# Optimization experiments

Measured on AMD Instinct MI355X. Metric: run time of the kernel, lower is better.

## Reference

```python
import jax, jax.numpy as jnp
import numpy as np

N_NODES = 50000
N_FEAT = 128
HID = 64
N_EDGES = 1600000
RK4_STEPS = 2
LN_EPS = 1e-5


def setup_inputs() -> dict:
    key = jax.random.key(0)
    ks = jax.random.split(key, 16)
    s = 1.0 / np.sqrt(HID)
    se = 1.0 / np.sqrt(N_FEAT)
    return {
        "x": jax.random.normal(ks[0], (N_NODES, N_FEAT), dtype=jnp.float32),
        "edge_index_pos": jax.random.randint(ks[1], (2, N_EDGES), 0, N_NODES, dtype=jnp.int64),
        "edge_index_neg": jax.random.randint(ks[2], (2, N_EDGES), 0, N_NODES, dtype=jnp.int64),
        "t": jnp.arange(2, dtype=jnp.float32),
        "W_enc": jax.random.uniform(ks[3], (HID, N_FEAT), jnp.float32, -se, se),
        "b_enc": jax.random.uniform(ks[4], (HID,), jnp.float32, -se, se),
        "W_pos": jax.random.uniform(ks[5], (HID, HID), jnp.float32, -s, s),
        "b_pos": jax.random.uniform(ks[6], (HID,), jnp.float32, -s, s),
        "W_neg": jax.random.uniform(ks[7], (HID, HID), jnp.float32, -s, s),
        "b_neg": jax.random.uniform(ks[8], (HID,), jnp.float32, -s, s),
        "W_psi_pos": jax.random.uniform(ks[9], (HID, HID), jnp.float32, -s, s),
        "b_psi_pos": jax.random.uniform(ks[10], (HID,), jnp.float32, -s, s),
        "W_psi_neg": jax.random.uniform(ks[11], (HID, HID), jnp.float32, -s, s),
        "b_psi_neg": jax.random.uniform(ks[12], (HID,), jnp.float32, -s, s),
        "ln_gamma": jnp.ones((HID,), jnp.float32),
        "ln_beta": jnp.zeros((HID,), jnp.float32),
    }


def _layer_norm(h, gamma, beta):
    mu = jnp.mean(h, axis=-1, keepdims=True)
    var = jnp.mean(jnp.square(h - mu), axis=-1, keepdims=True)
    return (h - mu) * jax.lax.rsqrt(var + LN_EPS) * gamma + beta


def _gcn_conv(h, W, b, src, dst, n_nodes):
    # PyG GCNConv: add self-loops, symmetric normalization D^-1/2 (A+I) D^-1/2 (X W^T) + b
    x = h @ W.T                                   # [N, HID]
    loops = jnp.arange(n_nodes, dtype=src.dtype)
    src_f = jnp.concatenate([src, loops])
    dst_f = jnp.concatenate([dst, loops])
    deg = jax.ops.segment_sum(jnp.ones_like(dst_f, dtype=x.dtype), dst_f, num_segments=n_nodes)
    dinv = jax.lax.rsqrt(deg)                     # deg >= 1 due to self-loops
    norm = dinv[src_f] * dinv[dst_f]              # [E+N]
    msg = norm[:, None] * x[src_f]                # gather
    return jax.ops.segment_sum(msg, dst_f, num_segments=n_nodes) + b


def _ode_func(h, ep, en, p):
    hn = _layer_norm(h, p["ln_gamma"], p["ln_beta"])
    h_pos = _gcn_conv(hn, p["W_pos"], p["b_pos"], ep[0], ep[1], hn.shape[0])
    h_neg = _gcn_conv(hn, p["W_neg"], p["b_neg"], en[0], en[1], hn.shape[0])
    # dropout is identity in eval mode
    delta = (h_pos @ p["W_psi_pos"].T + p["b_psi_pos"]) + (h_neg @ p["W_psi_neg"].T + p["b_psi_neg"])
    return jnp.clip(delta, -50.0, 50.0)


def reference(x, edge_index_pos, edge_index_neg, t,
              W_enc, b_enc, W_pos, b_pos, W_neg, b_neg,
              W_psi_pos, b_psi_pos, W_psi_neg, b_psi_neg, ln_gamma, ln_beta):
    p = dict(W_pos=W_pos, b_pos=b_pos, W_neg=W_neg, b_neg=b_neg,
             W_psi_pos=W_psi_pos, b_psi_pos=b_psi_pos, W_psi_neg=W_psi_neg,
             b_psi_neg=b_psi_neg, ln_gamma=ln_gamma, ln_beta=ln_beta)
    h = x @ W_enc.T + b_enc
    dt = (t[1] - t[0]) / RK4_STEPS
    f = lambda hh: _ode_func(hh, edge_index_pos, edge_index_neg, p)
    for _ in range(RK4_STEPS):  # fixed-step RK4 (stands in for odeint dopri5)
        k1 = f(h)
        k2 = f(h + 0.5 * dt * k1)
        k3 = f(h + 0.5 * dt * k2)
        k4 = f(h + dt * k3)
        h = h + (dt / 6.0) * (k1 + 2.0 * k2 + 2.0 * k3 + k4)
    return h
```

## Files before the change

### kernel.cpp

```cpp
#include <hip/hip_runtime.h>

#define N_NODES 50000
#define N_FEAT  128
#define HID     64
#define N_EDGES 1600000
#define LN_EPS  1e-5f
#define NB2     400
#define BW2     125
#define CAP2    5120u

typedef unsigned int uint;
typedef unsigned short ushort;
typedef _Float16 h2 __attribute__((ext_vector_type(2)));

#if __has_builtin(__builtin_amdgcn_fdot2)
#define FDOT2(a,b,c) __builtin_amdgcn_fdot2((a),(b),(c),false)
#else
#define FDOT2(a,b,c) ((float)(a)[0]*(float)(b)[0] + (float)(a)[1]*(float)(b)[1] + (c))
#endif

__device__ __forceinline__ float bcastf(float v, int l){
  return __uint_as_float(__builtin_amdgcn_readlane(__float_as_uint(v), l));
}
__device__ __forceinline__ h2 h2x(h2 a, int m){
  return __builtin_bit_cast(h2, __shfl_xor(__builtin_bit_cast(int, a), m));
}
__device__ __forceinline__ ushort f16u(float f){
  return __builtin_bit_cast(ushort, (_Float16)f);
}
__device__ __forceinline__ h2 wdup(uint e){
  return __builtin_bit_cast(h2, (e & 0xFFFF0000u) | (e >> 16));
}
__device__ __forceinline__ h2 wdup16(uint d){
  return __builtin_bit_cast(h2, d | (d << 16));
}
__device__ __forceinline__ void fma4(h2* a, uint4 v, h2 w){
  a[0] += w * __builtin_bit_cast(h2, v.x);
  a[1] += w * __builtin_bit_cast(h2, v.y);
  a[2] += w * __builtin_bit_cast(h2, v.z);
  a[3] += w * __builtin_bit_cast(h2, v.w);
}
__device__ __forceinline__ uint4 ldrow(const ushort* __restrict__ xs, uint r, int rowoff){
  return *(const uint4*)(xs + (size_t)r * HID + rowoff);
}

__global__ void prep_kernel(const float* __restrict__ Wpp, const float* __restrict__ Wp,
                            const float* __restrict__ Wpn, const float* __restrict__ Wn,
                            const float* __restrict__ bp, const float* __restrict__ bpp,
                            const float* __restrict__ bn, const float* __restrict__ bpn,
                            ushort* __restrict__ Wc16_p, ushort* __restrict__ Wc16_n,
                            float* __restrict__ bc,
                            ushort* __restrict__ hn16a, ushort* __restrict__ hn16b){
  int idx = blockIdx.x * blockDim.x + threadIdx.x;
  if (idx < 4096){
    int j = idx >> 6, k = idx & 63;
    float sp = 0.f, sn = 0.f;
    for (int m = 0; m < 64; ++m){
      sp += Wpp[j * 64 + m] * Wp[m * 64 + k];
      sn += Wpn[j * 64 + m] * Wn[m * 64 + k];
    }
    Wc16_p[idx] = f16u(sp); Wc16_n[idx] = f16u(sn);
  } else if (idx < 4160){
    int j = idx - 4096;
    float s = bpp[j] + bpn[j];
    for (int m = 0; m < 64; ++m) s += Wpp[j * 64 + m] * bp[m] + Wpn[j * 64 + m] * bn[m];
    bc[j] = s;
  } else if (idx < 4224){
    int q = idx - 4160;
    hn16a[(size_t)N_NODES * HID + q] = 0;
    hn16b[(size_t)N_NODES * HID + q] = 0;
  }
}

__global__ __launch_bounds__(256) void binA_kernel(
    const int* __restrict__ ep, const int* __restrict__ en,
    uint* __restrict__ bin_cur, uint* __restrict__ recs_p, uint* __restrict__ recs_n){
  __shared__ uint sh[8192];
  __shared__ uint cnt2[NB2], gb2[NB2], rnk2[NB2];
  const int NBLK = (N_EDGES + 8191) / 8192;
  int bid = blockIdx.x;
  int side = bid >= NBLK;
  const int* e = side ? en : ep;
  uint* recs = side ? recs_n : recs_p;
  uint* bcur = bin_cur + side * NB2;
  int cbase = (side ? bid - NBLK : bid) * 8192;
  int tid = threadIdx.x;
  for (int i = tid; i < NB2; i += 256){ cnt2[i] = 0; rnk2[i] = 0; }
  __syncthreads();
  for (int i = tid; i < 8192; i += 256){
    int t = cbase + i;
    uint r = 0xFFFFFFFFu;
    if (t < N_EDGES){
      uint s = (uint)e[t], d = (uint)e[N_EDGES + t];
      r = (d << 16) | s;
      atomicAdd(&cnt2[d / BW2], 1u);
    }
    sh[i] = r;
  }
  __syncthreads();
  for (int i = tid; i < NB2; i += 256) gb2[i] = atomicAdd(&bcur[i], cnt2[i]);
  __syncthreads();
  for (int i = tid; i < 8192; i += 256){
    uint r = sh[i];
    if (r != 0xFFFFFFFFu){
      uint b = (r >> 16) / BW2;
      uint pos = gb2[b] + atomicAdd(&rnk2[b], 1u);
      recs[b * CAP2 + pos] = r;
    }
  }
}

__global__ __launch_bounds__(256) void fillC_kernel(
    const uint* __restrict__ bin_cur,
    const uint* __restrict__ recs_p, const uint* __restrict__ recs_n,
    int* __restrict__ cnt_p, int* __restrict__ cnt_n,
    float* __restrict__ dinv_p, float* __restrict__ dinv_n,
    ushort* __restrict__ d16p, ushort* __restrict__ d16n,
    ushort* __restrict__ cs_p, ushort* __restrict__ cs_n){
  __shared__ int hist[128];
  __shared__ int curx[128];
  __shared__ ushort staged[CAP2];
  __shared__ uint base_s;
  int bid = blockIdx.x;
  int side = bid >= NB2; int b = side ? bid - NB2 : bid;
  const uint* recs = (side ? recs_n : recs_p) + (size_t)b * CAP2;
  int* cnt = side ? cnt_n : cnt_p;
  float* dinv = side ? dinv_n : dinv_p;
  ushort* d16 = side ? d16n : d16p;
  ushort* cs = side ? cs_n : cs_p;
  int tid = threadIdx.x, lane = tid & 63, wid = tid >> 6;
  int nodebase = b * BW2;
  if (tid < 128) hist[tid] = 0;
  __syncthreads();
  uint n = bin_cur[side * NB2 + b];
  if (wid == 1){
    uint s = 0;
    for (int k = lane; k < b; k += 64) s += bin_cur[side * NB2 + k];
    #pragma unroll
    for (int d = 1; d < 64; d <<= 1) s += __shfl_xor(s, d);
    if (lane == 0) base_s = s;
  }
  for (uint i = tid; i < n; i += 256)
    atomicAdd(&hist[(recs[i] >> 16) - nodebase], 1);
  __syncthreads();
  if (tid < BW2){
    int c = hist[tid];
    cnt[nodebase + tid] = c;
    float dv = rsqrtf((float)(c + 1));
    dinv[nodebase + tid] = dv;
    d16[nodebase + tid] = f16u(dv);
  }
  if (wid == 0){
    int carry = 0;
    #pragma unroll
    for (int base = 0; base < BW2; base += 64){
      int idx = base + lane;
      int v = (idx < BW2) ? hist[idx] : 0;
      int x = v;
      #pragma unroll
      for (int d = 1; d < 64; d <<= 1){
        int y = __shfl_up(x, d);
        if (lane >= d) x += y;
      }
      if (idx < BW2) curx[idx] = carry + x - v;
      int tot = __shfl(x, 63);
      carry = carry + tot;
    }
  }
  __syncthreads();
  for (uint i = tid; i < n; i += 256){
    uint r = recs[i];
    int d = (int)(r >> 16) - nodebase;
    int p = atomicAdd(&curx[d], 1);
    staged[p] = (ushort)(r & 0xFFFFu);
  }
  __syncthreads();
  uint base = base_s;
  for (uint i = tid; i < n; i += 256) cs[base + i] = staged[i];
}

__global__ __launch_bounds__(1024) void scan16_kernel(
    const uint* __restrict__ bin_cur,
    const int* __restrict__ c0, int* __restrict__ o0,
    const int* __restrict__ c1, int* __restrict__ o1){
  __shared__ int wsum[16];
  __shared__ int wexcl[16];
  __shared__ int carry_s;
  int side = blockIdx.x >> 3, b = blockIdx.x & 7;
  const int* c = side ? c1 : c0;
  int* o = side ? o1 : o0;
  int tid = threadIdx.x, lane = tid & 63, wid = tid >> 6;
  if (wid == 0){
    int s = 0;
    for (int k = lane; k < 50 * b; k += 64) s += (int)bin_cur[side * NB2 + k];
    #pragma unroll
    for (int d = 1; d < 64; d <<= 1) s += __shfl_xor(s, d);
    if (lane == 0) carry_s = s;
  }
  __syncthreads();
  int lo = b * 6250, hi = lo + 6250;
  for (int base = lo; base < hi; base += 1024){
    int idx = base + tid;
    int v = (idx < hi) ? c[idx] : 0;
    int x = v;
    #pragma unroll
    for (int d = 1; d < 64; d <<= 1){
      int y = __shfl_up(x, d);
      if (lane >= d) x += y;
    }
    if (lane == 63) wsum[wid] = x;
    __syncthreads();
    int block_total = 0;
    if (tid == 0){
      int s = 0;
      for (int wv = 0; wv < 16; ++wv){ wexcl[wv] = s; s += wsum[wv]; }
      block_total = s;
    }
    __syncthreads();
    if (idx < hi) o[idx] = carry_s + wexcl[wid] + (x - v);
    __syncthreads();
    if (tid == 0) carry_s += block_total;
    __syncthreads();
  }
  if (b == 7 && tid == 0) o[N_NODES] = carry_s;
}

__global__ __launch_bounds__(256) void pack_kernel(
    const ushort* __restrict__ cs_p, const ushort* __restrict__ cs_n,
    const ushort* __restrict__ d16p, const ushort* __restrict__ d16n,
    uint* __restrict__ cs32_p, uint* __restrict__ cs32_n){
  int i = blockIdx.x * 256 + threadIdx.x;
  if (i < N_EDGES){
    uint s = cs_p[i];
    cs32_p[i] = ((uint)d16p[s] << 16) | s;
  } else if (i < 2 * N_EDGES){
    int k = i - N_EDGES;
    uint s = cs_n[k];
    cs32_n[k] = ((uint)d16n[s] << 16) | s;
  }
}

__global__ __launch_bounds__(256) void enc_kernel(
    const float* __restrict__ x, const float* __restrict__ Wenc, const float* __restrict__ benc,
    const float* __restrict__ gamma, const float* __restrict__ beta,
    float* __restrict__ hbase, ushort* __restrict__ hn16){
  int lane = threadIdx.x & 63, wid = threadIdx.x >> 6;
  float we[128];
  const float* wr = Wenc + lane * N_FEAT;
  #pragma unroll
  for (int k4 = 0; k4 < 32; ++k4){
    float4 v = *(const float4*)(wr + 4 * k4);
    we[4*k4] = v.x; we[4*k4+1] = v.y; we[4*k4+2] = v.z; we[4*k4+3] = v.w;
  }
  float bv = benc[lane], g = gamma[lane], bt = beta[lane];
  int gw = blockIdx.x * 4 + wid, nw = gridDim.x * 4;
  for (int p = gw; p < N_NODES / 2; p += nw){
    int n0 = 2 * p, n1 = n0 + 1;
    float xa0 = x[(size_t)n0 * N_FEAT + lane], xb0 = x[(size_t)n0 * N_FEAT + 64 + lane];
    float xa1 = x[(size_t)n1 * N_FEAT + lane], xb1 = x[(size_t)n1 * N_FEAT + 64 + lane];
    float h0 = bv, h1 = bv;
    #pragma unroll
    for (int k = 0; k < 64; ++k){
      h0 += bcastf(xa0, k) * we[k];
      h1 += bcastf(xa1, k) * we[k];
      h0 += bcastf(xb0, k) * we[64 + k];
      h1 += bcastf(xb1, k) * we[64 + k];
    }
    hbase[n0 * HID + lane] = h0;
    hbase[n1 * HID + lane] = h1;
    float s0 = h0, q0 = h0 * h0, s1 = h1, q1 = h1 * h1;
    #pragma unroll
    for (int d = 1; d < 64; d <<= 1){
      s0 += __shfl_xor(s0, d); q0 += __shfl_xor(q0, d);
      s1 += __shfl_xor(s1, d); q1 += __shfl_xor(q1, d);
    }
    float mu0 = s0 * (1.0f/64.0f), var0 = q0 * (1.0f/64.0f) - mu0 * mu0;
    float mu1 = s1 * (1.0f/64.0f), var1 = q1 * (1.0f/64.0f) - mu1 * mu1;
    hn16[n0 * HID + lane] = f16u((h0 - mu0) * rsqrtf(var0 + LN_EPS) * g + bt);
    hn16[n1 * HID + lane] = f16u((h1 - mu1) * rsqrtf(var1 + LN_EPS) * g + bt);
  }
}

__device__ __forceinline__ void gather_side_acc(
    const ushort* __restrict__ hn16, const uint* __restrict__ cs32,
    int s0, int s1, int g, int rowoff, int lane, h2* acc){
  for (int base = s0; base < s1; base += 64){
    int jj = base + lane;
    uint e = (jj < s1) ? cs32[jj] : (uint)N_NODES;
    int cnt = min(64, s1 - base);
    int nt = (cnt + 7) >> 3;
    for (int t = 0; t < nt; ++t){
      uint ee = (uint)__shfl((int)e, 8 * t + g);
      fma4(acc, ldrow(hn16, ee & 0xFFFFu, rowoff), wdup(ee));
    }
  }
}

__global__ __launch_bounds__(256) void gather2_kernel(
    const ushort* __restrict__ hn16,
    const uint* __restrict__ cs32_p, const int* __restrict__ off_p,
    const float* __restrict__ dinv_p, const ushort* __restrict__ d16p,
    const uint* __restrict__ cs32_n, const int* __restrict__ off_n,
    const float* __restrict__ dinv_n, const ushort* __restrict__ d16n,
    const ushort* __restrict__ Wc16_p, const ushort* __restrict__ Wc16_n,
    const float* __restrict__ bc, const float* __restrict__ gamma, const float* __restrict__ beta,
    const float* __restrict__ tvec,
    float* __restrict__ hbase, float* __restrict__ acc, ushort* __restrict__ hn16o,
    int st, int emit){
  int lane = threadIdx.x & 63, wid = threadIdx.x >> 6;
  int pair = blockIdx.x * 4 + wid;
  int nA = 2 * pair, nB = nA + 1;
  if (nA >= N_NODES) return;
  int g = lane >> 3, rowoff = 8 * (lane & 7);

  int pA0 = off_p[nA], pA1 = off_p[nA + 1], pB1 = off_p[nB + 1];
  int qA0 = off_n[nA], qA1 = off_n[nA + 1], qB1 = off_n[nB + 1];
  int dPA = pA1 - pA0, dPB = pB1 - pA1, dNA = qA1 - qA0, dNB = qB1 - qA1;

  h2 aPA[4] = {h2{0,0},h2{0,0},h2{0,0},h2{0,0}};
  h2 aPB[4] = {h2{0,0},h2{0,0},h2{0,0},h2{0,0}};
  h2 aNA[4] = {h2{0,0},h2{0,0},h2{0,0},h2{0,0}};
  h2 aNB[4] = {h2{0,0},h2{0,0},h2{0,0},h2{0,0}};

  {
    uint4 rA = ldrow(hn16, (g==0)?(uint)nA:(uint)N_NODES, rowoff);
    uint4 rB = ldrow(hn16, (g==0)?(uint)nB:(uint)N_NODES, rowoff);
    uint dpA = d16p[nA], dnA = d16n[nA], dpB = d16p[nB], dnB = d16n[nB];
    fma4(aPA, rA, wdup16(dpA)); fma4(aNA, rA, wdup16(dnA));
    fma4(aPB, rB, wdup16(dpB)); fma4(aNB, rB, wdup16(dnB));
  }

  if (dPA <= 64 && dPB <= 64 && dNA <= 64 && dNB <= 64){
    uint ePA = (lane < dPA) ? cs32_p[pA0 + lane] : (uint)N_NODES;
    uint ePB = (lane < dPB) ? cs32_p[pA1 + lane] : (uint)N_NODES;
    uint eNA = (lane < dNA) ? cs32_n[qA0 + lane] : (uint)N_NODES;
    uint eNB = (lane < dNB) ? cs32_n[qA1 + lane] : (uint)N_NODES;
    int dP = dPA > dPB ? dPA : dPB;
    int dN = dNA > dNB ? dNA : dNB;
    int dM = dP > dN ? dP : dN;
    int ntM = (dM + 7) >> 3;
    for (int t = 0; t < ntM; t += 2){
      int gi0 = 8 * t + g, gi1 = gi0 + 8;
      uint uPA0 = (uint)__shfl((int)ePA, gi0), uPA1 = (uint)__shfl((int)ePA, gi1);
      uint uPB0 = (uint)__shfl((int)ePB, gi0), uPB1 = (uint)__shfl((int)ePB, gi1);
      uint uNA0 = (uint)__shfl((int)eNA, gi0), uNA1 = (uint)__shfl((int)eNA, gi1);
      uint uNB0 = (uint)__shfl((int)eNB, gi0), uNB1 = (uint)__shfl((int)eNB, gi1);
      uint4 vPA0 = ldrow(hn16, uPA0 & 0xFFFFu, rowoff);
      uint4 vPB0 = ldrow(hn16, uPB0 & 0xFFFFu, rowoff);
      uint4 vNA0 = ldrow(hn16, uNA0 & 0xFFFFu, rowoff);
      uint4 vNB0 = ldrow(hn16, uNB0 & 0xFFFFu, rowoff);
      uint4 vPA1 = ldrow(hn16, uPA1 & 0xFFFFu, rowoff);
      uint4 vPB1 = ldrow(hn16, uPB1 & 0xFFFFu, rowoff);
      uint4 vNA1 = ldrow(hn16, uNA1 & 0xFFFFu, rowoff);
      uint4 vNB1 = ldrow(hn16, uNB1 & 0xFFFFu, rowoff);
      fma4(aPA, vPA0, wdup(uPA0)); fma4(aPB, vPB0, wdup(uPB0));
      fma4(aNA, vNA0, wdup(uNA0)); fma4(aNB, vNB0, wdup(uNB0));
      fma4(aPA, vPA1, wdup(uPA1)); fma4(aPB, vPB1, wdup(uPB1));
      fma4(aNA, vNA1, wdup(uNA1)); fma4(aNB, vNB1, wdup(uNB1));
    }
  } else {
    gather_side_acc(hn16, cs32_p, pA0, pA1, g, rowoff, lane, aPA);
    gather_side_acc(hn16, cs32_p, pA1, pB1, g, rowoff, lane, aPB);
    gather_side_acc(hn16, cs32_n, qA0, qA1, g, rowoff, lane, aNA);
    gather_side_acc(hn16, cs32_n, qA1, qB1, g, rowoff, lane, aNB);
  }
  #pragma unroll
  for (int i = 0; i < 4; ++i){
    h2 a = aPA[i]; a += h2x(a, 8); a += h2x(a, 16); a += h2x(a, 32); aPA[i] = a;
    h2 b = aPB[i]; b += h2x(b, 8); b += h2x(b, 16); b += h2x(b, 32); aPB[i] = b;
    h2 c = aNA[i]; c += h2x(c, 8); c += h2x(c, 16); c += h2x(c, 32); aNA[i] = c;
    h2 d = aNB[i]; d += h2x(d, 8); d += h2x(d, 16); d += h2x(d, 32); aNB[i] = d;
  }

  float pAp[8], pAn[8], pBp[8], pBn[8];
  #pragma unroll
  for (int mh = 0; mh < 2; ++mh){
    uint4 wpc[4], wnc[4];
    #pragma unroll
    for (int m = 0; m < 4; ++m){
      int row = g * 8 + mh * 4 + m;
      wpc[m] = *(const uint4*)(Wc16_p + (size_t)row * HID + rowoff);
      wnc[m] = *(const uint4*)(Wc16_n + (size_t)row * HID + rowoff);
    }
    #pragma unroll
    for (int m = 0; m < 4; ++m){
      const uint* pu = (const uint*)&wpc[m];
      const uint* nu = (const uint*)&wnc[m];
      float sp = 0.f, sn = 0.f, tp = 0.f, tn = 0.f;
      #pragma unroll
      for (int i = 0; i < 4; ++i){
        h2 wph = __builtin_bit_cast(h2, pu[i]);
        h2 wnh = __builtin_bit_cast(h2, nu[i]);
        sp = FDOT2(aPA[i], wph, sp);
        sn = FDOT2(aNA[i], wnh, sn);
        tp = FDOT2(aPB[i], wph, tp);
        tn = FDOT2(aNB[i], wnh, tn);
      }
      pAp[mh*4+m] = sp; pAn[mh*4+m] = sn; pBp[mh*4+m] = tp; pBn[mh*4+m] = tn;
    }
  }

  int b0 = lane & 1, b1 = (lane >> 1) & 1, b2 = (lane >> 2) & 1;
  auto red8 = [&](float* p) -> float {
    float q[4];
    #pragma unroll
    for (int i = 0; i < 4; ++i){
      float a = p[2*i]     + __shfl_xor(p[2*i], 1);
      float b = p[2*i + 1] + __shfl_xor(p[2*i + 1], 1);
      q[i] = b0 ? b : a;
    }
    float r[2];
    #pragma unroll
    for (int u = 0; u < 2; ++u){
      float a = q[2*u]     + __shfl_xor(q[2*u], 2);
      float b = q[2*u + 1] + __shfl_xor(q[2*u + 1], 2);
      r[u] = b1 ? b : a;
    }
    float a = r[0] + __shfl_xor(r[0], 4);
    float b = r[1] + __shfl_xor(r[1], 4);
    return b2 ? b : a;
  };
  float mvAp = red8(pAp), mvAn = red8(pAn), mvBp = red8(pBp), mvBn = red8(pBn);

  int l = lane;
  float dvpA = dinv_p[nA], dvnA = dinv_n[nA], dvpB = dinv_p[nB], dvnB = dinv_n[nB];
  float bcl = bc[l];
  float dA = dvpA * mvAp + dvnA * mvAn + bcl;
  float dB = dvpB * mvBp + dvnB * mvBn + bcl;
  dA = fminf(fmaxf(dA, -50.f), 50.f);
  dB = fminf(fmaxf(dB, -50.f), 50.f);
  size_t ixA = (size_t)nA * HID + l, ixB = (size_t)nB * HID + l;
  float hbA = hbase[ixA], hbB = hbase[ixB];
  float avA = 0.f, avB = 0.f;
  if (st != 0){ avA = acc[ixA]; avB = acc[ixB]; }
  float dt = (tvec[1] - tvec[0]) * 0.5f;
  float hvA, hvB;
  if (st == 0){
    avA = dA; avB = dB;
    hvA = hbA + 0.5f * dt * dA; hvB = hbB + 0.5f * dt * dB;
  } else if (st == 1){
    avA += 2.0f * dA; avB += 2.0f * dB;
    hvA = hbA + 0.5f * dt * dA; hvB = hbB + 0.5f * dt * dB;
  } else if (st == 2){
    avA += 2.0f * dA; avB += 2.0f * dB;
    hvA = hbA + dt * dA; hvB = hbB + dt * dB;
  } else {
    hvA = hbA + (dt * (1.0f/6.0f)) * (avA + dA);
    hvB = hbB + (dt * (1.0f/6.0f)) * (avB + dB);
  }
  if (st < 3){
    acc[ixA] = avA; acc[ixB] = avB;
  } else {
    hbase[ixA] = hvA; hbase[ixB] = hvB;
  }
  if (emit){
    float sA = hvA, qA = hvA * hvA, sB = hvB, qB = hvB * hvB;
    #pragma unroll
    for (int d = 1; d < 64; d <<= 1){
      sA += __shfl_xor(sA, d); qA += __shfl_xor(qA, d);
      sB += __shfl_xor(sB, d); qB += __shfl_xor(qB, d);
    }
    float muA = sA * (1.0f/64.0f), varA = qA * (1.0f/64.0f) - muA * muA;
    float muB = sB * (1.0f/64.0f), varB = qB * (1.0f/64.0f) - muB * muB;
    float rsA = rsqrtf(varA + LN_EPS), rsB = rsqrtf(varB + LN_EPS);
    float gl = gamma[l], bl = beta[l];
    hn16o[ixA] = f16u((hvA - muA) * rsA * gl + bl);
    hn16o[ixB] = f16u((hvB - muB) * rsB * gl + bl);
  }
}

extern "C" void kernel_launch(void* const* d_in, const int* in_sizes, int n_in,
                              void* d_out, int out_size, void* d_ws, size_t ws_size,
                              hipStream_t stream){
  const float* x     = (const float*)d_in[0];
  const int*   ep    = (const int*)d_in[1];
  const int*   en    = (const int*)d_in[2];
  const float* tvec  = (const float*)d_in[3];
  const float* W_enc = (const float*)d_in[4];
  const float* b_enc = (const float*)d_in[5];
  const float* W_pos = (const float*)d_in[6];
  const float* b_pos = (const float*)d_in[7];
  const float* W_neg = (const float*)d_in[8];
  const float* b_neg = (const float*)d_in[9];
  const float* W_pp  = (const float*)d_in[10];
  const float* b_pp  = (const float*)d_in[11];
  const float* W_pn  = (const float*)d_in[12];
  const float* b_pn  = (const float*)d_in[13];
  const float* gamma = (const float*)d_in[14];
  const float* beta  = (const float*)d_in[15];
  float* hbase = (float*)d_out;

  char* w = (char*)d_ws;
  auto alloc = [&](size_t bytes) -> char* {
    char* p = w;
    w += (bytes + 255) & ~(size_t)255;
    return p;
  };
  uint*  bin_cur = (uint*)alloc(2 * NB2 * 4);
  int*   cnt_p = (int*)alloc(N_NODES * 4);
  int*   cnt_n = (int*)alloc(N_NODES * 4);
  int*   off_p = (int*)alloc((N_NODES + 1) * 4);
  int*   off_n = (int*)alloc((N_NODES + 1) * 4);
  float* dinv_p= (float*)alloc(N_NODES * 4);
  float* dinv_n= (float*)alloc(N_NODES * 4);
  ushort* d16p = (ushort*)alloc(N_NODES * 2);
  ushort* d16n = (ushort*)alloc(N_NODES * 2);
  uint*  recs_p= (uint*)alloc((size_t)NB2 * CAP2 * 4);
  uint*  recs_n= (uint*)alloc((size_t)NB2 * CAP2 * 4);
  ushort* cs_p = (ushort*)alloc((size_t)N_EDGES * 2);
  ushort* cs_n = (ushort*)alloc((size_t)N_EDGES * 2);
  ushort* hn16a= (ushort*)alloc((size_t)(N_NODES + 1) * HID * 2);
  ushort* hn16b= (ushort*)alloc((size_t)(N_NODES + 1) * HID * 2);
  float* accb  = (float*)alloc((size_t)N_NODES * HID * 4);
  ushort* Wc16_p = (ushort*)alloc(HID * HID * 2);
  ushort* Wc16_n = (ushort*)alloc(HID * HID * 2);
  float* bc    = (float*)alloc(HID * 4);
  uint* cs32_p = recs_p;
  uint* cs32_n = recs_n;

  hipMemsetAsync(bin_cur, 0, 2 * NB2 * 4, stream);

  dim3 blk(256);
  const int NBLK_A = 2 * ((N_EDGES + 8191) / 8192);
  prep_kernel<<<17, blk, 0, stream>>>(W_pp, W_pos, W_pn, W_neg, b_pos, b_pp, b_neg, b_pn,
                                      Wc16_p, Wc16_n, bc, hn16a, hn16b);
  binA_kernel<<<NBLK_A, blk, 0, stream>>>(ep, en, bin_cur, recs_p, recs_n);
  fillC_kernel<<<2 * NB2, blk, 0, stream>>>(bin_cur, recs_p, recs_n,
                                            cnt_p, cnt_n, dinv_p, dinv_n,
                                            d16p, d16n, cs_p, cs_n);
  scan16_kernel<<<16, 1024, 0, stream>>>(bin_cur, cnt_p, off_p, cnt_n, off_n);
  pack_kernel<<<(2 * N_EDGES + 255) / 256, blk, 0, stream>>>(cs_p, cs_n, d16p, d16n,
                                                             cs32_p, cs32_n);
  enc_kernel<<<1024, blk, 0, stream>>>(x, W_enc, b_enc, gamma, beta, hbase, hn16a);

  for (int s = 0; s < 8; ++s){
    ushort* rd = (s & 1) ? hn16b : hn16a;
    ushort* wr2 = (s & 1) ? hn16a : hn16b;
    gather2_kernel<<<(N_NODES / 2 + 3) / 4, blk, 0, stream>>>(
        rd, cs32_p, off_p, dinv_p, d16p, cs32_n, off_n, dinv_n, d16n,
        Wc16_p, Wc16_n, bc, gamma, beta, tvec, hbase, accb, wr2,
        s & 3, (s < 7) ? 1 : 0);
  }
}
```

Before: 652.2 us.

## Fuse eight RK4 stage launches into one cooperative persistent kernel

Replaces the eight per-stage gather kernel launches with a single cooperative kernel of 1024 blocks that loops over the stages, separating them with grid-wide syncs. Each wave keeps its nodes' base state and RK accumulator in shared memory, so those are no longer read from and written to global memory every stage. The stage body is factored into a shared device function, and the old multi-launch path stays as a fallback when occupancy is too low or the cooperative launch fails. In exchange it adds grid-barrier cost, a fixed grid that each wave covers in up to 7 passes, and about 28 KB of shared memory per block, which may limit occupancy.

```diff
diff --git a/kernel.cpp b/kernel.cpp
--- a/kernel.cpp
+++ b/kernel.cpp
@@ -1,4 +1,7 @@
 #include <hip/hip_runtime.h>
+#include <hip/hip_cooperative_groups.h>
+
+namespace cg = cooperative_groups;
 
 #define N_NODES 50000
 #define N_FEAT  128
@@ -8,6 +11,8 @@
 #define NB2     400
 #define BW2     125
 #define CAP2    5120u
+#define GRID_C  1024
+#define NPASS   7
 
 typedef unsigned int uint;
 typedef unsigned short ushort;
@@ -296,6 +301,164 @@
   }
 }
 
+__device__ __forceinline__ void stage_body(
+    const ushort* __restrict__ rd, ushort* __restrict__ wr,
+    const uint* __restrict__ cs32_p, const int* __restrict__ off_p,
+    const float* __restrict__ dinv_p, const ushort* __restrict__ d16p,
+    const uint* __restrict__ cs32_n, const int* __restrict__ off_n,
+    const float* __restrict__ dinv_n, const ushort* __restrict__ d16n,
+    const ushort* __restrict__ Wc16_p, const ushort* __restrict__ Wc16_n,
+    const float* __restrict__ bc, const float* __restrict__ gamma,
+    const float* __restrict__ beta, float dt, int st, int emit,
+    int nA, int nB, int lane, int g, int rowoff,
+    float& hbA, float& hbB, float& avA, float& avB){
+  int pA0 = off_p[nA], pA1 = off_p[nA + 1], pB1 = off_p[nB + 1];
+  int qA0 = off_n[nA], qA1 = off_n[nA + 1], qB1 = off_n[nB + 1];
+  int dPA = pA1 - pA0, dPB = pB1 - pA1, dNA = qA1 - qA0, dNB = qB1 - qA1;
+
+  h2 aPA[4] = {h2{0,0},h2{0,0},h2{0,0},h2{0,0}};
+  h2 aPB[4] = {h2{0,0},h2{0,0},h2{0,0},h2{0,0}};
+  h2 aNA[4] = {h2{0,0},h2{0,0},h2{0,0},h2{0,0}};
+  h2 aNB[4] = {h2{0,0},h2{0,0},h2{0,0},h2{0,0}};
+
+  {
+    uint4 rA = ldrow(rd, (g==0)?(uint)nA:(uint)N_NODES, rowoff);
+    uint4 rB = ldrow(rd, (g==0)?(uint)nB:(uint)N_NODES, rowoff);
+    uint dpA = d16p[nA], dnA = d16n[nA], dpB = d16p[nB], dnB = d16n[nB];
+    fma4(aPA, rA, wdup16(dpA)); fma4(aNA, rA, wdup16(dnA));
+    fma4(aPB, rB, wdup16(dpB)); fma4(aNB, rB, wdup16(dnB));
+  }
+
+  if (dPA <= 64 && dPB <= 64 && dNA <= 64 && dNB <= 64){
+    uint ePA = (lane < dPA) ? cs32_p[pA0 + lane] : (uint)N_NODES;
+    uint ePB = (lane < dPB) ? cs32_p[pA1 + lane] : (uint)N_NODES;
+    uint eNA = (lane < dNA) ? cs32_n[qA0 + lane] : (uint)N_NODES;
+    uint eNB = (lane < dNB) ? cs32_n[qA1 + lane] : (uint)N_NODES;
+    int dP = dPA > dPB ? dPA : dPB;
+    int dN = dNA > dNB ? dNA : dNB;
+    int dM = dP > dN ? dP : dN;
+    int ntM = (dM + 7) >> 3;
+    for (int t = 0; t < ntM; t += 2){
+      int gi0 = 8 * t + g, gi1 = gi0 + 8;
+      uint uPA0 = (uint)__shfl((int)ePA, gi0), uPA1 = (uint)__shfl((int)ePA, gi1);
+      uint uPB0 = (uint)__shfl((int)ePB, gi0), uPB1 = (uint)__shfl((int)ePB, gi1);
+      uint uNA0 = (uint)__shfl((int)eNA, gi0), uNA1 = (uint)__shfl((int)eNA, gi1);
+      uint uNB0 = (uint)__shfl((int)eNB, gi0), uNB1 = (uint)__shfl((int)eNB, gi1);
+      uint4 vPA0 = ldrow(rd, uPA0 & 0xFFFFu, rowoff);
+      uint4 vPB0 = ldrow(rd, uPB0 & 0xFFFFu, rowoff);
+      uint4 vNA0 = ldrow(rd, uNA0 & 0xFFFFu, rowoff);
+      uint4 vNB0 = ldrow(rd, uNB0 & 0xFFFFu, rowoff);
+      uint4 vPA1 = ldrow(rd, uPA1 & 0xFFFFu, rowoff);
+      uint4 vPB1 = ldrow(rd, uPB1 & 0xFFFFu, rowoff);
+      uint4 vNA1 = ldrow(rd, uNA1 & 0xFFFFu, rowoff);
+      uint4 vNB1 = ldrow(rd, uNB1 & 0xFFFFu, rowoff);
+      fma4(aPA, vPA0, wdup(uPA0)); fma4(aPB, vPB0, wdup(uPB0));
+      fma4(aNA, vNA0, wdup(uNA0)); fma4(aNB, vNB0, wdup(uNB0));
+      fma4(aPA, vPA1, wdup(uPA1)); fma4(aPB, vPB1, wdup(uPB1));
+      fma4(aNA, vNA1, wdup(uNA1)); fma4(aNB, vNB1, wdup(uNB1));
+    }
+  } else {
+    gather_side_acc(rd, cs32_p, pA0, pA1, g, rowoff, lane, aPA);
+    gather_side_acc(rd, cs32_p, pA1, pB1, g, rowoff, lane, aPB);
+    gather_side_acc(rd, cs32_n, qA0, qA1, g, rowoff, lane, aNA);
+    gather_side_acc(rd, cs32_n, qA1, qB1, g, rowoff, lane, aNB);
+  }
+  #pragma unroll
+  for (int i = 0; i < 4; ++i){
+    h2 a = aPA[i]; a += h2x(a, 8); a += h2x(a, 16); a += h2x(a, 32); aPA[i] = a;
+    h2 b = aPB[i]; b += h2x(b, 8); b += h2x(b, 16); b += h2x(b, 32); aPB[i] = b;
+    h2 c = aNA[i]; c += h2x(c, 8); c += h2x(c, 16); c += h2x(c, 32); aNA[i] = c;
+    h2 d = aNB[i]; d += h2x(d, 8); d += h2x(d, 16); d += h2x(d, 32); aNB[i] = d;
+  }
+
+  float pAp[8], pAn[8], pBp[8], pBn[8];
+  #pragma unroll
+  for (int mh = 0; mh < 2; ++mh){
+    uint4 wpc[4], wnc[4];
+    #pragma unroll
+    for (int m = 0; m < 4; ++m){
+      int row = g * 8 + mh * 4 + m;
+      wpc[m] = *(const uint4*)(Wc16_p + (size_t)row * HID + rowoff);
+      wnc[m] = *(const uint4*)(Wc16_n + (size_t)row * HID + rowoff);
+    }
+    #pragma unroll
+    for (int m = 0; m < 4; ++m){
+      const uint* pu = (const uint*)&wpc[m];
+      const uint* nu = (const uint*)&wnc[m];
+      float sp = 0.f, sn = 0.f, tp = 0.f, tn = 0.f;
+      #pragma unroll
+      for (int i = 0; i < 4; ++i){
+        h2 wph = __builtin_bit_cast(h2, pu[i]);
+        h2 wnh = __builtin_bit_cast(h2, nu[i]);
+        sp = FDOT2(aPA[i], wph, sp);
+        sn = FDOT2(aNA[i], wnh, sn);
+        tp = FDOT2(aPB[i], wph, tp);
+        tn = FDOT2(aNB[i], wnh, tn);
+      }
+      pAp[mh*4+m] = sp; pAn[mh*4+m] = sn; pBp[mh*4+m] = tp; pBn[mh*4+m] = tn;
+    }
+  }
+
+  int b0 = lane & 1, b1 = (lane >> 1) & 1, b2 = (lane >> 2) & 1;
+  auto red8 = [&](float* p) -> float {
+    float q[4];
+    #pragma unroll
+    for (int i = 0; i < 4; ++i){
+      float a = p[2*i]     + __shfl_xor(p[2*i], 1);
+      float b = p[2*i + 1] + __shfl_xor(p[2*i + 1], 1);
+      q[i] = b0 ? b : a;
+    }
+    float r[2];
+    #pragma unroll
+    for (int u = 0; u < 2; ++u){
+      float a = q[2*u]     + __shfl_xor(q[2*u], 2);
+      float b = q[2*u + 1] + __shfl_xor(q[2*u + 1], 2);
+      r[u] = b1 ? b : a;
+    }
+    float a = r[0] + __shfl_xor(r[0], 4);
+    float b = r[1] + __shfl_xor(r[1], 4);
+    return b2 ? b : a;
+  };
+  float mvAp = red8(pAp), mvAn = red8(pAn), mvBp = red8(pBp), mvBn = red8(pBn);
+
+  int l = lane;
+  float dvpA = dinv_p[nA], dvnA = dinv_n[nA], dvpB = dinv_p[nB], dvnB = dinv_n[nB];
+  float bcl = bc[l];
+  float dA = dvpA * mvAp + dvnA * mvAn + bcl;
+  float dB = dvpB * mvBp + dvnB * mvBn + bcl;
+  dA = fminf(fmaxf(dA, -50.f), 50.f);
+  dB = fminf(fmaxf(dB, -50.f), 50.f);
+  float hvA, hvB;
+  if (st == 0){
+    avA = dA; avB = dB;
+    hvA = hbA + 0.5f * dt * dA; hvB = hbB + 0.5f * dt * dB;
+  } else if (st == 1){
+    avA += 2.0f * dA; avB += 2.0f * dB;
+    hvA = hbA + 0.5f * dt * dA; hvB = hbB + 0.5f * dt * dB;
+  } else if (st == 2){
+    avA += 2.0f * dA; avB += 2.0f * dB;
+    hvA = hbA + dt * dA; hvB = hbB + dt * dB;
+  } else {
+    hvA = hbA + (dt * (1.0f/6.0f)) * (avA + dA);
+    hvB = hbB + (dt * (1.0f/6.0f)) * (avB + dB);
+    hbA = hvA; hbB = hvB;
+  }
+  if (emit){
+    float sA = hvA, qA = hvA * hvA, sB = hvB, qB = hvB * hvB;
+    #pragma unroll
+    for (int d = 1; d < 64; d <<= 1){
+      sA += __shfl_xor(sA, d); qA += __shfl_xor(qA, d);
+      sB += __shfl_xor(sB, d); qB += __shfl_xor(qB, d);
+    }
+    float muA = sA * (1.0f/64.0f), varA = qA * (1.0f/64.0f) - muA * muA;
+    float muB = sB * (1.0f/64.0f), varB = qB * (1.0f/64.0f) - muB * muB;
+    float rsA = rsqrtf(varA + LN_EPS), rsB = rsqrtf(varB + LN_EPS);
+    float gl = gamma[l], bl = beta[l];
+    wr[(size_t)nA * HID + l] = f16u((hvA - muA) * rsA * gl + bl);
+    wr[(size_t)nB * HID + l] = f16u((hvB - muB) * rsB * gl + bl);
+  }
+}
+
 __global__ __launch_bounds__(256) void gather2_kernel(
     const ushort* __restrict__ hn16,
     const uint* __restrict__ cs32_p, const int* __restrict__ off_p,
@@ -312,160 +475,81 @@
   int nA = 2 * pair, nB = nA + 1;
   if (nA >= N_NODES) return;
   int g = lane >> 3, rowoff = 8 * (lane & 7);
-
-  int pA0 = off_p[nA], pA1 = off_p[nA + 1], pB1 = off_p[nB + 1];
-  int qA0 = off_n[nA], qA1 = off_n[nA + 1], qB1 = off_n[nB + 1];
-  int dPA = pA1 - pA0, dPB = pB1 - pA1, dNA = qA1 - qA0, dNB = qB1 - qA1;
-
-  h2 aPA[4] = {h2{0,0},h2{0,0},h2{0,0},h2{0,0}};
-  h2 aPB[4] = {h2{0,0},h2{0,0},h2{0,0},h2{0,0}};
-  h2 aNA[4] = {h2{0,0},h2{0,0},h2{0,0},h2{0,0}};
-  h2 aNB[4] = {h2{0,0},h2{0,0},h2{0,0},h2{0,0}};
-
-  {
-    uint4 rA = ldrow(hn16, (g==0)?(uint)nA:(uint)N_NODES, rowoff);
-    uint4 rB = ldrow(hn16, (g==0)?(uint)nB:(uint)N_NODES, rowoff);
-    uint dpA = d16p[nA], dnA = d16n[nA], dpB = d16p[nB], dnB = d16n[nB];
-    fma4(aPA, rA, wdup16(dpA)); fma4(aNA, rA, wdup16(dnA));
-    fma4(aPB, rB, wdup16(dpB)); fma4(aNB, rB, wdup16(dnB));
-  }
-
-  if (dPA <= 64 && dPB <= 64 && dNA <= 64 && dNB <= 64){
-    uint ePA = (lane < dPA) ? cs32_p[pA0 + lane] : (uint)N_NODES;
-    uint ePB = (lane < dPB) ? cs32_p[pA1 + lane] : (uint)N_NODES;
-    uint eNA = (lane < dNA) ? cs32_n[qA0 + lane] : (uint)N_NODES;
-    uint eNB = (lane < dNB) ? cs32_n[qA1 + lane] : (uint)N_NODES;
-    int dP = dPA > dPB ? dPA : dPB;
-    int dN = dNA > dNB ? dNA : dNB;
-    int dM = dP > dN ? dP : dN;
-    int ntM = (dM + 7) >> 3;
-    for (int t = 0; t < ntM; t += 2){
-      int gi0 = 8 * t + g, gi1 = gi0 + 8;
-      uint uPA0 = (uint)__shfl((int)ePA, gi0), uPA1 = (uint)__shfl((int)ePA, gi1);
-      uint uPB0 = (uint)__shfl((int)ePB, gi0), uPB1 = (uint)__shfl((int)ePB, gi1);
-      uint uNA0 = (uint)__shfl((int)eNA, gi0), uNA1 = (uint)__shfl((int)eNA, gi1);
-      uint uNB0 = (uint)__shfl((int)eNB, gi0), uNB1 = (uint)__shfl((int)eNB, gi1);
-      uint4 vPA0 = ldrow(hn16, uPA0 & 0xFFFFu, rowoff);
-      uint4 vPB0 = ldrow(hn16, uPB0 & 0xFFFFu, rowoff);
-      uint4 vNA0 = ldrow(hn16, uNA0 & 0xFFFFu, rowoff);
-      uint4 vNB0 = ldrow(hn16, uNB0 & 0xFFFFu, rowoff);
-      uint4 vPA1 = ldrow(hn16, uPA1 & 0xFFFFu, rowoff);
-      uint4 vPB1 = ldrow(hn16, uPB1 & 0xFFFFu, rowoff);
-      uint4 vNA1 = ldrow(hn16, uNA1 & 0xFFFFu, rowoff);
-      uint4 vNB1 = ldrow(hn16, uNB1 & 0xFFFFu, rowoff);
-      fma4(aPA, vPA0, wdup(uPA0)); fma4(aPB, vPB0, wdup(uPB0));
-      fma4(aNA, vNA0, wdup(uNA0)); fma4(aNB, vNB0, wdup(uNB0));
-      fma4(aPA, vPA1, wdup(uPA1)); fma4(aPB, vPB1, wdup(uPB1));
-      fma4(aNA, vNA1, wdup(uNA1)); fma4(aNB, vNB1, wdup(uNB1));
-    }
-  } else {
-    gather_side_acc(hn16, cs32_p, pA0, pA1, g, rowoff, lane, aPA);
-    gather_side_acc(hn16, cs32_p, pA1, pB1, g, rowoff, lane, aPB);
-    gather_side_acc(hn16, cs32_n, qA0, qA1, g, rowoff, lane, aNA);
-    gather_side_acc(hn16, cs32_n, qA1, qB1, g, rowoff, lane, aNB);
-  }
-  #pragma unroll
-  for (int i = 0; i < 4; ++i){
-    h2 a = aPA[i]; a += h2x(a, 8); a += h2x(a, 16); a += h2x(a, 32); aPA[i] = a;
-    h2 b = aPB[i]; b += h2x(b, 8); b += h2x(b, 16); b += h2x(b, 32); aPB[i] = b;
-    h2 c = aNA[i]; c += h2x(c, 8); c += h2x(c, 16); c += h2x(c, 32); aNA[i] = c;
-    h2 d = aNB[i]; d += h2x(d, 8); d += h2x(d, 16); d += h2x(d, 32); aNB[i] = d;
-  }
-
-  float pAp[8], pAn[8], pBp[8], pBn[8];
-  #pragma unroll
-  for (int mh = 0; mh < 2; ++mh){
-    uint4 wpc[4], wnc[4];
-    #pragma unroll
-    for (int m = 0; m < 4; ++m){
-      int row = g * 8 + mh * 4 + m;
-      wpc[m] = *(const uint4*)(Wc16_p + (size_t)row * HID + rowoff);
-      wnc[m] = *(const uint4*)(Wc16_n + (size_t)row * HID + rowoff);
-    }
-    #pragma unroll
-    for (int m = 0; m < 4; ++m){
-      const uint* pu = (const uint*)&wpc[m];
-      const uint* nu = (const uint*)&wnc[m];
-      float sp = 0.f, sn = 0.f, tp = 0.f, tn = 0.f;
-      #pragma unroll
-      for (int i = 0; i < 4; ++i){
-        h2 wph = __builtin_bit_cast(h2, pu[i]);
-        h2 wnh = __builtin_bit_cast(h2, nu[i]);
-        sp = FDOT2(aPA[i], wph, sp);
-        sn = FDOT2(aNA[i], wnh, sn);
-        tp = FDOT2(aPB[i], wph, tp);
-        tn = FDOT2(aNB[i], wnh, tn);
-      }
-      pAp[mh*4+m] = sp; pAn[mh*4+m] = sn; pBp[mh*4+m] = tp; pBn[mh*4+m] = tn;
-    }
-  }
-
-  int b0 = lane & 1, b1 = (lane >> 1) & 1, b2 = (lane >> 2) & 1;
-  auto red8 = [&](float* p) -> float {
-    float q[4];
-    #pragma unroll
-    for (int i = 0; i < 4; ++i){
-      float a = p[2*i]     + __shfl_xor(p[2*i], 1);
-      float b = p[2*i + 1] + __shfl_xor(p[2*i + 1], 1);
-      q[i] = b0 ? b : a;
-    }
-    float r[2];
-    #pragma unroll
-    for (int u = 0; u < 2; ++u){
-      float a = q[2*u]     + __shfl_xor(q[2*u], 2);
-      float b = q[2*u + 1] + __shfl_xor(q[2*u + 1], 2);
-      r[u] = b1 ? b : a;
-    }
-    float a = r[0] + __shfl_xor(r[0], 4);
-    float b = r[1] + __shfl_xor(r[1], 4);
-    return b2 ? b : a;
-  };
-  float mvAp = red8(pAp), mvAn = red8(pAn), mvBp = red8(pBp), mvBn = red8(pBn);
-
-  int l = lane;
-  float dvpA = dinv_p[nA], dvnA = dinv_n[nA], dvpB = dinv_p[nB], dvnB = dinv_n[nB];
-  float bcl = bc[l];
-  float dA = dvpA * mvAp + dvnA * mvAn + bcl;
-  float dB = dvpB * mvBp + dvnB * mvBn + bcl;
-  dA = fminf(fmaxf(dA, -50.f), 50.f);
-  dB = fminf(fmaxf(dB, -50.f), 50.f);
-  size_t ixA = (size_t)nA * HID + l, ixB = (size_t)nB * HID + l;
+  size_t ixA = (size_t)nA * HID + lane, ixB = (size_t)nB * HID + lane;
   float hbA = hbase[ixA], hbB = hbase[ixB];
   float avA = 0.f, avB = 0.f;
   if (st != 0){ avA = acc[ixA]; avB = acc[ixB]; }
   float dt = (tvec[1] - tvec[0]) * 0.5f;
-  float hvA, hvB;
-  if (st == 0){
-    avA = dA; avB = dB;
-    hvA = hbA + 0.5f * dt * dA; hvB = hbB + 0.5f * dt * dB;
-  } else if (st == 1){
-    avA += 2.0f * dA; avB += 2.0f * dB;
-    hvA = hbA + 0.5f * dt * dA; hvB = hbB + 0.5f * dt * dB;
-  } else if (st == 2){
-    avA += 2.0f * dA; avB += 2.0f * dB;
-    hvA = hbA + dt * dA; hvB = hbB + dt * dB;
-  } else {
-    hvA = hbA + (dt * (1.0f/6.0f)) * (avA + dA);
-    hvB = hbB + (dt * (1.0f/6.0f)) * (avB + dB);
-  }
+  stage_body(hn16, hn16o, cs32_p, off_p, dinv_p, d16p, cs32_n, off_n, dinv_n, d16n,
+             Wc16_p, Wc16_n, bc, gamma, beta, dt, st, emit,
+             nA, nB, lane, g, rowoff, hbA, hbB, avA, avB);
   if (st < 3){
     acc[ixA] = avA; acc[ixB] = avB;
   } else {
-    hbase[ixA] = hvA; hbase[ixB] = hvB;
-  }
-  if (emit){
-    float sA = hvA, qA = hvA * hvA, sB = hvB, qB = hvB * hvB;
-    #pragma unroll
-    for (int d = 1; d < 64; d <<= 1){
-      sA += __shfl_xor(sA, d); qA += __shfl_xor(qA, d);
-      sB += __shfl_xor(sB, d); qB += __shfl_xor(qB, d);
-    }
-    float muA = sA * (1.0f/64.0f), varA = qA * (1.0f/64.0f) - muA * muA;
-    float muB = sB * (1.0f/64.0f), varB = qB * (1.0f/64.0f) - muB * muB;
-    float rsA = rsqrtf(varA + LN_EPS), rsB = rsqrtf(varB + LN_EPS);
-    float gl = gamma[l], bl = beta[l];
-    hn16o[ixA] = f16u((hvA - muA) * rsA * gl + bl);
-    hn16o[ixB] = f16u((hvB - muB) * rsB * gl + bl);
+    hbase[ixA] = hbA; hbase[ixB] = hbB;
+  }
+}
+
+__global__ __launch_bounds__(256, 4) void rk_coop(
+    ushort* __restrict__ hn16a, ushort* __restrict__ hn16b,
+    const uint* __restrict__ cs32_p, const int* __restrict__ off_p,
+    const float* __restrict__ dinv_p, const ushort* __restrict__ d16p,
+    const uint* __restrict__ cs32_n, const int* __restrict__ off_n,
+    const float* __restrict__ dinv_n, const ushort* __restrict__ d16n,
+    const ushort* __restrict__ Wc16_p, const ushort* __restrict__ Wc16_n,
+    const float* __restrict__ bc, const float* __restrict__ gamma,
+    const float* __restrict__ beta, const float* __restrict__ tvec,
+    float* __restrict__ hbase){
+  __shared__ float stf[4 * NPASS * 4 * 64];
+  cg::grid_group gridg = cg::this_grid();
+  int lane = threadIdx.x & 63, wid = threadIdx.x >> 6;
+  int g = lane >> 3, rowoff = 8 * (lane & 7);
+  const int WSLOTS = GRID_C * 4;
+
+  for (int ps = 0; ps < NPASS; ++ps){
+    int pair = blockIdx.x * 4 + wid + ps * WSLOTS;
+    if (pair < N_NODES / 2){
+      int sb = (wid * NPASS + ps) * 256 + lane;
+      stf[sb]      = hbase[(size_t)(2 * pair) * HID + lane];
+      stf[sb + 64] = hbase[(size_t)(2 * pair + 1) * HID + lane];
+    }
+  }
+  float dt = (tvec[1] - tvec[0]) * 0.5f;
+
+  for (int s = 0; s < 8; ++s){
+    const ushort* rd = (s & 1) ? hn16b : hn16a;
+    ushort* wr = (s & 1) ? hn16a : hn16b;
+    int st = s & 3, emit = (s < 7) ? 1 : 0;
+    for (int ps = 0; ps < NPASS; ++ps){
+      int pair = blockIdx.x * 4 + wid + ps * WSLOTS;
+      if (pair < N_NODES / 2){
+        int nA = 2 * pair, nB = nA + 1;
+        int sb = (wid * NPASS + ps) * 256 + lane;
+        float hbA = stf[sb], hbB = stf[sb + 64];
+        float avA = 0.f, avB = 0.f;
+        if (st != 0){ avA = stf[sb + 128]; avB = stf[sb + 192]; }
+        stage_body(rd, wr, cs32_p, off_p, dinv_p, d16p, cs32_n, off_n, dinv_n, d16n,
+                   Wc16_p, Wc16_n, bc, gamma, beta, dt, st, emit,
+                   nA, nB, lane, g, rowoff, hbA, hbB, avA, avB);
+        if (st < 3){
+          stf[sb + 128] = avA; stf[sb + 192] = avB;
+        } else {
+          stf[sb] = hbA; stf[sb + 64] = hbB;
+        }
+      }
+    }
+    __threadfence();
+    gridg.sync();
+    __threadfence();
+  }
+
+  for (int ps = 0; ps < NPASS; ++ps){
+    int pair = blockIdx.x * 4 + wid + ps * WSLOTS;
+    if (pair < N_NODES / 2){
+      int sb = (wid * NPASS + ps) * 256 + lane;
+      hbase[(size_t)(2 * pair) * HID + lane]     = stf[sb];
+      hbase[(size_t)(2 * pair + 1) * HID + lane] = stf[sb + 64];
+    }
   }
 }
 
@@ -533,12 +617,31 @@
                                                              cs32_p, cs32_n);
   enc_kernel<<<1024, blk, 0, stream>>>(x, W_enc, b_enc, gamma, beta, hbase, hn16a);
 
-  for (int s = 0; s < 8; ++s){
-    ushort* rd = (s & 1) ? hn16b : hn16a;
-    ushort* wr2 = (s & 1) ? hn16a : hn16b;
-    gather2_kernel<<<(N_NODES / 2 + 3) / 4, blk, 0, stream>>>(
-        rd, cs32_p, off_p, dinv_p, d16p, cs32_n, off_n, dinv_n, d16n,
-        Wc16_p, Wc16_n, bc, gamma, beta, tvec, hbase, accb, wr2,
-        s & 3, (s < 7) ? 1 : 0);
-  }
-}
+  int maxBlocksPerCU = 0;
+  hipError_t qerr = hipOccupancyMaxActiveBlocksPerMultiprocessor(
+      &maxBlocksPerCU, (const void*)rk_coop, 256, 0);
+  bool coop_ok = (qerr == hipSuccess) && (maxBlocksPerCU >= 4);
+
+  if (coop_ok){
+    void* args[] = {
+      (void*)&hn16a, (void*)&hn16b,
+      (void*)&cs32_p, (void*)&off_p, (void*)&dinv_p, (void*)&d16p,
+      (void*)&cs32_n, (void*)&off_n, (void*)&dinv_n, (void*)&d16n,
+      (void*)&Wc16_p, (void*)&Wc16_n, (void*)&bc, (void*)&gamma, (void*)&beta,
+      (void*)&tvec, (void*)&hbase
+    };
+    hipError_t lerr = hipLaunchCooperativeKernel((const void*)rk_coop, dim3(GRID_C),
+                                                 dim3(256), args, 0, stream);
+    coop_ok = (lerr == hipSuccess);
+  }
+  if (!coop_ok){
+    for (int s = 0; s < 8; ++s){
+      ushort* rd2 = (s & 1) ? hn16b : hn16a;
+      ushort* wr2 = (s & 1) ? hn16a : hn16b;
+      gather2_kernel<<<(N_NODES / 2 + 3) / 4, blk, 0, stream>>>(
+          rd2, cs32_p, off_p, dinv_p, d16p, cs32_n, off_n, dinv_n, d16n,
+          Wc16_p, Wc16_n, bc, gamma, beta, tvec, hbase, accb, wr2,
+          s & 3, (s < 7) ? 1 : 0);
+    }
+  }
+}
```

New measurement: 706.4 us. 8.3% more time.
